# Optimization experiments

Hardware: AMD Instinct MI355X
Metric: run time of the kernel (lower is better)

The kernel has to match this reference:

```python
import jax, jax.numpy as jnp
import numpy as np

Q, N, H, C, L = 512, 1000, 1024, 128, 8  # questions, students, hidden, concepts, lstm layers
LAM, GUESS = 10.0, 0.25  # self.l and guess_prob


def setup_inputs() -> dict:
    key = jax.random.key(0)
    ks = jax.random.split(key, 12)
    def w(k, shape, fan):
        return (jax.random.uniform(k, shape, jnp.float32, -1.0, 1.0) / np.sqrt(fan)).astype(jnp.float32)
    return {
        "inputs": jax.random.normal(ks[0], (Q, N), jnp.float32),
        "concept_col": jax.random.randint(ks[1], (Q,), 0, C),  # concepts[1][i]
        "W_inp": w(ks[2], (H, N), N),
        "b_inp": jnp.zeros((H,), jnp.float32),
        "W_ih0": w(ks[3], (4 * N, H), H),
        "W_hh0": w(ks[4], (4 * N, N), N),
        "b_ih0": jnp.zeros((4 * N,), jnp.float32),
        "b_hh0": jnp.zeros((4 * N,), jnp.float32),
        "W_ih": w(ks[5], (L - 1, 4 * N, N), N),
        "W_hh": w(ks[6], (L - 1, 4 * N, N), N),
        "b_ih": jnp.zeros((L - 1, 4 * N), jnp.float32),
        "b_hh": jnp.zeros((L - 1, 4 * N), jnp.float32),
        "W_lin": w(ks[7], (C,), 1),  # Linear(1, C) weight, shape [C]
        "b_lin": jnp.zeros((C,), jnp.float32),
        "D_nz": 0.1 * jax.random.normal(ks[8], (Q,), jnp.float32),  # D[concepts]
    }


def _cell(Wih, Whh, bih, bhh, x, h, c):
    # PyTorch LSTM cell, gate order i,f,g,o
    g = Wih @ x + bih + Whh @ h + bhh
    i, f, gg, o = jnp.split(g, 4)
    i, f, o = jax.nn.sigmoid(i), jax.nn.sigmoid(f), jax.nn.sigmoid(o)
    c = f * c + i * jnp.tanh(gg)
    return o * jnp.tanh(c), c


def _forward(inputs, concept_col, W_inp, b_inp, W_ih0, W_hh0, b_ih0, b_hh0,
             W_ih, W_hh, b_ih, b_hh, W_lin, b_lin, D_nz):
    def step(carry, xs):
        h, c, ssum = carry  # h,c: [L,N]
        x_row, cc, d = xs
        x = W_inp @ x_row + b_inp  # [H]
        hs, cs = [], []
        hl, cl = _cell(W_ih0, W_hh0, b_ih0, b_hh0, x, h[0], c[0])
        hs.append(hl); cs.append(cl)
        for l in range(L - 1):
            hl, cl = _cell(W_ih[l], W_hh[l], b_ih[l], b_hh[l], hl, h[l + 1], c[l + 1])
            hs.append(hl); cs.append(cl)
        skills = hl[:, None] * W_lin[None, :] + b_lin  # [N, C]
        skills = (skills - skills.min()) / (skills.max() - skills.min())  # global min-max
        out = jnp.maximum(GUESS, 1.0 - jnp.exp(-LAM * (skills[:, cc] - d)))  # floored_exp_irf, [N]
        return (jnp.stack(hs), jnp.stack(cs), ssum + skills), out

    h0 = jnp.zeros((L, N), inputs.dtype)
    c0 = jnp.zeros((L, N), inputs.dtype)
    s0 = jnp.zeros((N, C), inputs.dtype)
    (h, c, ssum), outputs = jax.lax.scan(step, (h0, c0, s0), (inputs, concept_col, D_nz))
    return outputs, ssum / Q  # outputs [Q,N], averaged skills [N,C]


def reference(inputs, concept_col, W_inp, b_inp, W_ih0, W_hh0, b_ih0, b_hh0,
              W_ih, W_hh, b_ih, b_hh, W_lin, b_lin, D_nz):
    return _forward(inputs, concept_col, W_inp, b_inp, W_ih0, W_hh0, b_ih0, b_hh0,
                    W_ih, W_hh, b_ih, b_hh, W_lin, b_lin, D_nz)
```

## Files before the change

kernel.cpp:

```cpp
#include <hip/hip_runtime.h>
#include <math.h>

#define QQ 512
#define NN 1000
#define HHID 1024
#define HPAD 1024
#define CCON 128
#define G4 4000
#define LAYERS 8
#define TC 64
#define CHUNKS (QQ / TC)
#define CONC 4
#define LBLK 63
#define MAXSTG 32

typedef unsigned long long ull;

__device__ inline float wred_min(float v){ for(int o=32;o;o>>=1) v=fminf(v,__shfl_xor(v,o)); return v; }
__device__ inline float wred_max(float v){ for(int o=32;o;o>>=1) v=fmaxf(v,__shfl_xor(v,o)); return v; }
__device__ inline float wred_sum(float v){ for(int o=32;o;o>>=1) v+=__shfl_xor(v,o); return v; }

__global__ __launch_bounds__(256) void gemm_nt(
    const float* __restrict__ A, const float* __restrict__ B,
    const float* __restrict__ bias1,
    float* __restrict__ C, int M, int K, int R, int lda, int ldc) {
  __shared__ float As[16][65];
  __shared__ float Bs[16][65];
  int tid = threadIdx.x;
  int tx = tid & 15, ty = tid >> 4;
  int m0 = blockIdx.y * 64, r0 = blockIdx.x * 64;
  float acc[4][4] = {};
  for (int k0 = 0; k0 < K; k0 += 16) {
#pragma unroll
    for (int i = 0; i < 4; i++) {
      int idx = tid + 256 * i;
      int ml = idx >> 4, kl = idx & 15;
      int m = m0 + ml, k = k0 + kl;
      As[kl][ml] = (m < M && k < K) ? A[(size_t)m * lda + k] : 0.f;
      int r = r0 + ml;
      Bs[kl][ml] = (r < R && k < K) ? B[(size_t)r * K + k] : 0.f;
    }
    __syncthreads();
#pragma unroll
    for (int kk = 0; kk < 16; kk++) {
      float a[4], b[4];
#pragma unroll
      for (int i = 0; i < 4; i++) a[i] = As[kk][ty * 4 + i];
#pragma unroll
      for (int j = 0; j < 4; j++) b[j] = Bs[kk][tx * 4 + j];
#pragma unroll
      for (int i = 0; i < 4; i++)
#pragma unroll
        for (int j = 0; j < 4; j++) acc[i][j] += a[i] * b[j];
    }
    __syncthreads();
  }
#pragma unroll
  for (int i = 0; i < 4; i++) {
    int m = m0 + ty * 4 + i;
    if (m >= M) continue;
#pragma unroll
    for (int j = 0; j < 4; j++) {
      int r = r0 + tx * 4 + j;
      if (r >= R) continue;
      float v = acc[i][j];
      if (bias1) v += bias1[r];
      C[(size_t)m * ldc + r] = v;
    }
  }
}

struct PArgs {
  const float* X;
  const float* Wih0; const float* Whh0; const float* bih0; const float* bhh0;
  const float* Wih7; const float* Whh7; const float* bih7; const float* bhh7;
  ull* Hall; ull* Call64;
  int nstages;
  int pl[MAXSTG * CONC]; int pc[MAXSTG * CONC];
};

__global__ __launch_bounds__(1024, 4) void lstm_persist(PArgs a) {
  __shared__ __align__(16) float As[64][68];
  __shared__ __align__(16) float Bs[64][68];
  __shared__ float gl[TC * 64];
  __shared__ float hs[2][1024];
  int blkid = blockIdx.x;
  int lanePair = blockIdx.y;
  int tid = threadIdx.x;
  int wave = tid >> 6, lane = tid & 63;
  int n = blkid * 16 + wave;
  bool active = (n < NN);

  if (tid >= NN) { hs[0][tid] = 0.f; hs[1][tid] = 0.f; }
  __syncthreads();

  for (int s = 0; s < a.nstages; s++) {
    int l = a.pl[s * CONC + lanePair];
    if (l < 0) continue;
    int c = a.pc[s * CONC + lanePair];
    int t0 = c * TC;
    int kin = (l == 0) ? HHID : NN;
    const float* Wih = (l == 0) ? a.Wih0 : a.Wih7 + (size_t)(l - 1) * G4 * NN;
    const float* Whh = (l == 0) ? a.Whh0 : a.Whh7 + (size_t)(l - 1) * G4 * NN;
    const float* b1  = (l == 0) ? a.bih0 : a.bih7 + (size_t)(l - 1) * G4;
    const float* b2  = (l == 0) ? a.bhh0 : a.bhh7 + (size_t)(l - 1) * G4;
    const ull* Hin64 = a.Hall + (size_t)(l - 1) * QQ * HPAD;
    ull* Hout64 = a.Hall + (size_t)l * QQ * HPAD;
    ull* CallL = a.Call64 + (size_t)l * HPAD;

    if (l > 0) {
      if (tid < NN) {
        const ull* gp = &Hin64[(size_t)(t0 + TC - 1) * HPAD + tid];
        while ((unsigned)(__hip_atomic_load(gp, __ATOMIC_RELAXED,
                                            __HIP_MEMORY_SCOPE_AGENT) >> 32)
               != (unsigned)(t0 + TC))
          __builtin_amdgcn_s_sleep(8);
      }
      __syncthreads();
    }

    {
      int ttA = tid >> 4;
      int w16 = tid & 15;
      int nn = blkid * 16 + w16;
      float accq[4] = {0.f, 0.f, 0.f, 0.f};
      float pbq[4];
#pragma unroll
      for (int q = 0; q < 4; q++)
        pbq[q] = (nn < NN) ? b1[q * NN + nn] + b2[q * NN + nn] : 0.f;
      int ldr = tid >> 4, ldc4 = tid & 15;
      int qb = ldr >> 4, nb = blkid * 16 + (ldr & 15);
      for (int k0 = 0; k0 < kin; k0 += 64) {
        int k = k0 + ldc4 * 4;
        float4 av;
        if (l == 0) {
          av = *(const float4*)&a.X[(size_t)(t0 + ldr) * HPAD + k];
        } else {
          float f0 = 0.f, f1 = 0.f, f2 = 0.f, f3 = 0.f;
          const ull* rowp = &Hin64[(size_t)(t0 + ldr) * HPAD];
          if (k < kin)
            f0 = __uint_as_float((unsigned)__hip_atomic_load(
                &rowp[k], __ATOMIC_RELAXED, __HIP_MEMORY_SCOPE_AGENT));
          if (k + 1 < kin)
            f1 = __uint_as_float((unsigned)__hip_atomic_load(
                &rowp[k + 1], __ATOMIC_RELAXED, __HIP_MEMORY_SCOPE_AGENT));
          if (k + 2 < kin)
            f2 = __uint_as_float((unsigned)__hip_atomic_load(
                &rowp[k + 2], __ATOMIC_RELAXED, __HIP_MEMORY_SCOPE_AGENT));
          if (k + 3 < kin)
            f3 = __uint_as_float((unsigned)__hip_atomic_load(
                &rowp[k + 3], __ATOMIC_RELAXED, __HIP_MEMORY_SCOPE_AGENT));
          av.x = f0; av.y = f1; av.z = f2; av.w = f3;
        }
        *(float4*)&As[ldr][ldc4 * 4] = av;
        float4 bv = {0.f, 0.f, 0.f, 0.f};
        if (nb < NN) {
          if (k + 3 < kin) {
            bv = *(const float4*)&Wih[(size_t)(qb * NN + nb) * kin + k];
          } else {
            float* f = (float*)&bv;
#pragma unroll
            for (int e = 0; e < 4; e++)
              if (k + e < kin) f[e] = Wih[(size_t)(qb * NN + nb) * kin + k + e];
          }
        }
        *(float4*)&Bs[ldr][ldc4 * 4] = bv;
        __syncthreads();
#pragma unroll
        for (int kk = 0; kk < 64; kk += 4) {
          float4 aa = *(const float4*)&As[ttA][kk];
#pragma unroll
          for (int q = 0; q < 4; q++) {
            float4 b = *(const float4*)&Bs[q * 16 + w16][kk];
            accq[q] += aa.x * b.x + aa.y * b.y + aa.z * b.z + aa.w * b.w;
          }
        }
        __syncthreads();
      }
#pragma unroll
      for (int q = 0; q < 4; q++)
        gl[ttA * 64 + q * 16 + w16] = accq[q] + pbq[q];
    }

    float wreg[4][16];
    if (active) {
#pragma unroll
      for (int q = 0; q < 4; q++) {
        const float* wr = Whh + (size_t)(q * NN + n) * NN;
#pragma unroll
        for (int it = 0; it < 16; it++) {
          int k = it * 64 + lane;
          wreg[q][it] = (k < NN) ? wr[k] : 0.f;
        }
      }
    } else {
#pragma unroll
      for (int q = 0; q < 4; q++)
#pragma unroll
        for (int it = 0; it < 16; it++) wreg[q][it] = 0.f;
    }
#pragma unroll
    for (int q = 0; q < 4; q++)
#pragma unroll
      for (int it = 0; it < 16; it++)
        asm volatile("" : "+v"(wreg[q][it]));

    __syncthreads();

    float creg = 0.f;
    if (t0 > 0 && active) {
      const ull* cp = &CallL[n];
      for (;;) {
        ull v = __hip_atomic_load(cp, __ATOMIC_RELAXED,
                                  __HIP_MEMORY_SCOPE_AGENT);
        if ((unsigned)(v >> 32) == (unsigned)c) {
          creg = __uint_as_float((unsigned)v);
          break;
        }
        __builtin_amdgcn_s_sleep(2);
      }
    }

    for (int tt = 0; tt < TC; tt++) {
      int t = t0 + tt;
      float* hb = hs[t & 1];
      if (t > 0 && tid < NN) {
        const ull* src = Hout64 + (size_t)(t - 1) * HPAD + tid;
        for (;;) {
          ull v = __hip_atomic_load(src, __ATOMIC_RELAXED,
                                    __HIP_MEMORY_SCOPE_AGENT);
          if ((unsigned)(v >> 32) == (unsigned)t) {
            hb[tid] = __uint_as_float((unsigned)v);
            break;
          }
          __builtin_amdgcn_s_sleep(1);
        }
      }
      __syncthreads();
      if (active) {
        float g0 = gl[tt * 64 + wave];
        float g1 = gl[tt * 64 + 16 + wave];
        float g2 = gl[tt * 64 + 32 + wave];
        float g3 = gl[tt * 64 + 48 + wave];
        if (t > 0) {
          float a0 = 0.f, a1 = 0.f, a2 = 0.f, a3 = 0.f;
#pragma unroll
          for (int it = 0; it < 16; it++) {
            float hv = hb[it * 64 + lane];
            a0 += wreg[0][it] * hv;
            a1 += wreg[1][it] * hv;
            a2 += wreg[2][it] * hv;
            a3 += wreg[3][it] * hv;
          }
#pragma unroll
          for (int o = 32; o; o >>= 1) {
            a0 += __shfl_xor(a0, o);
            a1 += __shfl_xor(a1, o);
            a2 += __shfl_xor(a2, o);
            a3 += __shfl_xor(a3, o);
          }
          g0 += a0; g1 += a1; g2 += a2; g3 += a3;
        }
        float ii = 1.f / (1.f + expf(-g0));
        float ff = 1.f / (1.f + expf(-g1));
        float gg = tanhf(g2);
        float oo = 1.f / (1.f + expf(-g3));
        creg = ff * creg + ii * gg;
        float h = oo * tanhf(creg);
        if (lane == 0) {
          ull pkt = ((ull)(unsigned)(t + 1) << 32) | (ull)__float_as_uint(h);
          __hip_atomic_store(&Hout64[(size_t)t * HPAD + n], pkt,
                             __ATOMIC_RELAXED, __HIP_MEMORY_SCOPE_AGENT);
        }
      }
    }
    if (active && lane == 0) {
      ull pkt = ((ull)(unsigned)(c + 1) << 32) | (ull)__float_as_uint(creg);
      __hip_atomic_store(&CallL[n], pkt, __ATOMIC_RELAXED,
                         __HIP_MEMORY_SCOPE_AGENT);
    }
    __syncthreads();
  }
}

__global__ __launch_bounds__(256) void epilogue_out(
    const ull* __restrict__ H7,
    const float* __restrict__ Wlin, const float* __restrict__ blin,
    const int* __restrict__ ccol, const float* __restrict__ Dnz,
    float* __restrict__ out,
    float* __restrict__ irbuf, float* __restrict__ mnirbuf) {
  int t = blockIdx.x, tid = threadIdx.x;
  int wave = tid >> 6, lane = tid & 63;
  __shared__ float hbuf[NN];
  __shared__ float smin[4], smax[4];
  __shared__ float bc[2];
  float lmin = 3.4e38f, lmax = -3.4e38f;
  for (int i = tid; i < NN; i += 256) {
    float v = __uint_as_float((unsigned)H7[(size_t)t * HPAD + i]);
    hbuf[i] = v;
    lmin = fminf(lmin, v); lmax = fmaxf(lmax, v);
  }
  lmin = wred_min(lmin); lmax = wred_max(lmax);
  if (lane == 0) { smin[wave] = lmin; smax[wave] = lmax; }
  __syncthreads();
  if (tid == 0) {
    bc[0] = fminf(fminf(smin[0], smin[1]), fminf(smin[2], smin[3]));
    bc[1] = fmaxf(fmaxf(smax[0], smax[1]), fmaxf(smax[2], smax[3]));
  }
  __syncthreads();
  float hmn = bc[0], hmx = bc[1];
  float clo = 3.4e38f, chi = -3.4e38f;
  if (tid < CCON) {
    float w = Wlin[tid], b = blin[tid];
    clo = b + fminf(w * hmn, w * hmx);
    chi = b + fmaxf(w * hmn, w * hmx);
  }
  clo = wred_min(clo); chi = wred_max(chi);
  __syncthreads();
  if (lane == 0) { smin[wave] = clo; smax[wave] = chi; }
  __syncthreads();
  if (tid == 0) {
    float mn = fminf(fminf(smin[0], smin[1]), fminf(smin[2], smin[3]));
    float mx = fmaxf(fmaxf(smax[0], smax[1]), fmaxf(smax[2], smax[3]));
    float ir = 1.f / (mx - mn);
    bc[0] = mn; bc[1] = ir;
    irbuf[t] = ir;
    mnirbuf[t] = mn * ir;
  }
  __syncthreads();
  float mn = bc[0], ir = bc[1];
  int cc = ccol[t];
  float wcc = Wlin[cc], bcc = blin[cc], d = Dnz[t];
  for (int n = tid; n < NN; n += 256) {
    float s = (hbuf[n] * wcc + bcc - mn) * ir;
    out[(size_t)t * NN + n] = fmaxf(0.25f, 1.f - expf(-10.f * (s - d)));
  }
}

__global__ void reduce_scalars(const float* __restrict__ ir,
                               const float* __restrict__ mnir,
                               float* __restrict__ scal) {
  int tid = threadIdx.x;
  int wave = tid >> 6, lane = tid & 63;
  __shared__ float s1[8], s2[8];
  float a = ir[tid], b = mnir[tid];
  a = wred_sum(a); b = wred_sum(b);
  if (lane == 0) { s1[wave] = a; s2[wave] = b; }
  __syncthreads();
  if (tid == 0) {
    float A = 0.f, B = 0.f;
    for (int i = 0; i < 8; i++) { A += s1[i]; B += s2[i]; }
    scal[0] = A; scal[1] = B;
  }
}

__global__ void accum_A(const ull* __restrict__ H7,
                        const float* __restrict__ ir,
                        float* __restrict__ Avec) {
  int n = blockIdx.x * 256 + threadIdx.x;
  if (n < NN) {
    float acc = 0.f;
    for (int t = 0; t < QQ; t++)
      acc += __uint_as_float((unsigned)H7[(size_t)t * HPAD + n]) * ir[t];
    Avec[n] = acc;
  }
}

__global__ void skills_out(const float* __restrict__ Avec,
                           const float* __restrict__ Wlin,
                           const float* __restrict__ blin,
                           const float* __restrict__ scal,
                           float* __restrict__ out) {
  int idx = blockIdx.x * 256 + threadIdx.x;
  if (idx < NN * CCON) {
    int n = idx >> 7, c = idx & 127;
    out[idx] = (Wlin[c] * Avec[n] + blin[c] * scal[0] - scal[1]) * (1.f / (float)QQ);
  }
}

extern "C" void kernel_launch(void* const* d_in, const int* in_sizes, int n_in,
                              void* d_out, int out_size, void* d_ws, size_t ws_size,
                              hipStream_t stream) {
  const float* inputs = (const float*)d_in[0];
  const int*   ccol   = (const int*)d_in[1];
  const float* W_inp  = (const float*)d_in[2];
  const float* b_inp  = (const float*)d_in[3];
  const float* W_ih0  = (const float*)d_in[4];
  const float* W_hh0  = (const float*)d_in[5];
  const float* b_ih0  = (const float*)d_in[6];
  const float* b_hh0  = (const float*)d_in[7];
  const float* W_ih   = (const float*)d_in[8];
  const float* W_hh   = (const float*)d_in[9];
  const float* b_ih   = (const float*)d_in[10];
  const float* b_hh   = (const float*)d_in[11];
  const float* W_lin  = (const float*)d_in[12];
  const float* b_lin  = (const float*)d_in[13];
  const float* D_nz   = (const float*)d_in[14];

  float* ws = (float*)d_ws;
  float* X     = ws;
  ull*   Hall  = (ull*)(X + (size_t)QQ * HPAD);
  ull*   Call64 = Hall + (size_t)LAYERS * QQ * HPAD;
  float* tail  = (float*)(Call64 + (size_t)LAYERS * HPAD);
  float* irb   = tail;
  float* mnir  = irb + QQ;
  float* Avec  = mnir + QQ;
  float* scal  = Avec + 1024;

  float* out_main   = (float*)d_out;
  float* out_skills = (float*)d_out + QQ * NN;

  hipMemsetAsync(Hall, 0,
                 ((size_t)LAYERS * QQ * HPAD + LAYERS * HPAD) * sizeof(ull),
                 stream);

  gemm_nt<<<dim3(HPAD / 64, QQ / 64), 256, 0, stream>>>(
      inputs, W_inp, b_inp, X, QQ, NN, HPAD, NN, HPAD);

  PArgs pa;
  pa.X = X;
  pa.Wih0 = W_ih0; pa.Whh0 = W_hh0; pa.bih0 = b_ih0; pa.bhh0 = b_hh0;
  pa.Wih7 = W_ih; pa.Whh7 = W_hh; pa.bih7 = b_ih; pa.bhh7 = b_hh;
  pa.Hall = Hall; pa.Call64 = Call64;
  for (int i = 0; i < MAXSTG * CONC; i++) { pa.pl[i] = -1; pa.pc[i] = -1; }
  {
    bool donep[LAYERS][CHUNKS] = {};
    int remaining = LAYERS * CHUNKS;
    int s = 0;
    while (remaining > 0 && s < MAXSTG) {
      bool sel[LAYERS][CHUNKS] = {};
      int np = 0;
      int spl[CONC], spc[CONC];
      for (int pick = 0; pick < CONC; pick++) {
        int bl = -1, bc = -1, bkey = 1 << 30;
        for (int l = 0; l < LAYERS; l++)
          for (int c = 0; c < CHUNKS; c++) {
            if (donep[l][c] || sel[l][c]) continue;
            if (l > 0 && !donep[l - 1][c]) continue;
            if (c > 0 && !donep[l][c - 1]) continue;
            int key = (l + c) * 16 + (LAYERS - 1 - l);
            if (key < bkey) { bkey = key; bl = l; bc = c; }
          }
        if (bl < 0) break;
        sel[bl][bc] = true; spl[np] = bl; spc[np] = bc; np++;
      }
      for (int i = 0; i < np; i++) {
        pa.pl[s * CONC + i] = spl[i];
        pa.pc[s * CONC + i] = spc[i];
        donep[spl[i]][spc[i]] = true;
      }
      remaining -= np;
      s++;
    }
    pa.nstages = s;
  }
  lstm_persist<<<dim3(LBLK, CONC), 1024, 0, stream>>>(pa);

  const ull* H7 = Hall + (size_t)7 * QQ * HPAD;
  epilogue_out<<<QQ, 256, 0, stream>>>(H7, W_lin, b_lin, ccol, D_nz,
                                       out_main, irb, mnir);
  reduce_scalars<<<1, 512, 0, stream>>>(irb, mnir, scal);
  accum_A<<<4, 256, 0, stream>>>(H7, irb, Avec);
  skills_out<<<(NN * CCON) / 256, 256, 0, stream>>>(Avec, W_lin, b_lin, scal,
                                                    out_skills);
}
```

Before: 7.200 ms.

## Replace host-planned wavefront schedule with fixed layer-to-lane assignment

Drops the host-computed stage table that assigned (layer, chunk) tiles to four block lanes. Each lane now owns layers j and j+4 and walks all chunks in order, so the cell state stays in a register and the Call64 handoff buffer and its memset go away. The input projection is split into two 32-row halves that each wait only for their own rows of the previous layer, which lets a layer start sooner. The trade-off is that only half the threads do FMAs in the projection and the fixed pairing of layers may leave lanes idle during pipeline fill and drain.

New measurement: 8.220 ms. 14.2% more time.

```diff
diff --git a/kernel.cpp b/kernel.cpp
--- a/kernel.cpp
+++ b/kernel.cpp
@@ -10,9 +10,8 @@
 #define LAYERS 8
 #define TC 64
 #define CHUNKS (QQ / TC)
-#define CONC 4
+#define NLANE 4
 #define LBLK 63
-#define MAXSTG 32
 
 typedef unsigned long long ull;
 
@@ -74,18 +73,16 @@
   const float* X;
   const float* Wih0; const float* Whh0; const float* bih0; const float* bhh0;
   const float* Wih7; const float* Whh7; const float* bih7; const float* bhh7;
-  ull* Hall; ull* Call64;
-  int nstages;
-  int pl[MAXSTG * CONC]; int pc[MAXSTG * CONC];
+  ull* Hall;
 };
 
-__global__ __launch_bounds__(1024, 4) void lstm_persist(PArgs a) {
-  __shared__ __align__(16) float As[64][68];
+__global__ __launch_bounds__(1024, 4) void lstm_resident(PArgs a) {
+  __shared__ __align__(16) float As[32][68];
   __shared__ __align__(16) float Bs[64][68];
   __shared__ float gl[TC * 64];
   __shared__ float hs[2][1024];
+  int j = blockIdx.y;
   int blkid = blockIdx.x;
-  int lanePair = blockIdx.y;
   int tid = threadIdx.x;
   int wave = tid >> 6, lane = tid & 63;
   int n = blkid * 16 + wave;
@@ -94,11 +91,10 @@
   if (tid >= NN) { hs[0][tid] = 0.f; hs[1][tid] = 0.f; }
   __syncthreads();
 
-  for (int s = 0; s < a.nstages; s++) {
-    int l = a.pl[s * CONC + lanePair];
-    if (l < 0) continue;
-    int c = a.pc[s * CONC + lanePair];
-    int t0 = c * TC;
+  float creg = 0.f;
+
+  for (int seq = 0; seq < 2; seq++) {
+    int l = j + 4 * seq;
     int kin = (l == 0) ? HHID : NN;
     const float* Wih = (l == 0) ? a.Wih0 : a.Wih7 + (size_t)(l - 1) * G4 * NN;
     const float* Whh = (l == 0) ? a.Whh0 : a.Whh7 + (size_t)(l - 1) * G4 * NN;
@@ -106,180 +102,170 @@
     const float* b2  = (l == 0) ? a.bhh0 : a.bhh7 + (size_t)(l - 1) * G4;
     const ull* Hin64 = a.Hall + (size_t)(l - 1) * QQ * HPAD;
     ull* Hout64 = a.Hall + (size_t)l * QQ * HPAD;
-    ull* CallL = a.Call64 + (size_t)l * HPAD;
-
-    if (l > 0) {
-      if (tid < NN) {
-        const ull* gp = &Hin64[(size_t)(t0 + TC - 1) * HPAD + tid];
-        while ((unsigned)(__hip_atomic_load(gp, __ATOMIC_RELAXED,
-                                            __HIP_MEMORY_SCOPE_AGENT) >> 32)
-               != (unsigned)(t0 + TC))
-          __builtin_amdgcn_s_sleep(8);
+
+    for (int c = 0; c < CHUNKS; c++) {
+      int t0 = c * TC;
+      if (c == 0) creg = 0.f;
+
+      for (int g = 0; g < 2; g++) {
+        int r0 = t0 + 32 * g;
+        if (l > 0) {
+          if (tid < NN) {
+            const ull* gp = &Hin64[(size_t)(r0 + 31) * HPAD + tid];
+            while ((unsigned)(__hip_atomic_load(gp, __ATOMIC_RELAXED,
+                                                __HIP_MEMORY_SCOPE_AGENT) >> 32)
+                   != (unsigned)(r0 + 32))
+              __builtin_amdgcn_s_sleep(4);
+          }
+          __syncthreads();
+        }
+        int ttA = tid >> 4;
+        int w16 = tid & 15;
+        bool act = (tid < 512);
+        int nn = blkid * 16 + w16;
+        float accq[4] = {0.f, 0.f, 0.f, 0.f};
+        float pbq[4];
+#pragma unroll
+        for (int q = 0; q < 4; q++)
+          pbq[q] = (nn < NN) ? b1[q * NN + nn] + b2[q * NN + nn] : 0.f;
+        int arow = tid >> 5, ac2 = (tid & 31) * 2;
+        int brow = tid >> 4, bc4 = (tid & 15) * 4;
+        int qb = brow >> 4, nb = blkid * 16 + (brow & 15);
+        for (int k0 = 0; k0 < kin; k0 += 64) {
+          if (l == 0) {
+            const float* rowp = &a.X[(size_t)(r0 + arow) * HPAD + k0];
+            As[arow][ac2]     = rowp[ac2];
+            As[arow][ac2 + 1] = rowp[ac2 + 1];
+          } else {
+            const ull* rowp = &Hin64[(size_t)(r0 + arow) * HPAD + k0];
+            int ka = k0 + ac2;
+            As[arow][ac2] = (ka < kin)
+                ? __uint_as_float((unsigned)__hip_atomic_load(
+                      &rowp[ac2], __ATOMIC_RELAXED, __HIP_MEMORY_SCOPE_AGENT))
+                : 0.f;
+            As[arow][ac2 + 1] = (ka + 1 < kin)
+                ? __uint_as_float((unsigned)__hip_atomic_load(
+                      &rowp[ac2 + 1], __ATOMIC_RELAXED,
+                      __HIP_MEMORY_SCOPE_AGENT))
+                : 0.f;
+          }
+          {
+            int k = k0 + bc4;
+            float4 bv = {0.f, 0.f, 0.f, 0.f};
+            if (nb < NN) {
+              if (k + 3 < kin) {
+                bv = *(const float4*)&Wih[(size_t)(qb * NN + nb) * kin + k];
+              } else {
+                float* f = (float*)&bv;
+#pragma unroll
+                for (int e = 0; e < 4; e++)
+                  if (k + e < kin)
+                    f[e] = Wih[(size_t)(qb * NN + nb) * kin + k + e];
+              }
+            }
+            *(float4*)&Bs[brow][bc4] = bv;
+          }
+          __syncthreads();
+          if (act) {
+#pragma unroll
+            for (int kk = 0; kk < 64; kk += 4) {
+              float4 av = *(const float4*)&As[ttA][kk];
+#pragma unroll
+              for (int q = 0; q < 4; q++) {
+                float4 b = *(const float4*)&Bs[q * 16 + w16][kk];
+                accq[q] += av.x * b.x + av.y * b.y + av.z * b.z + av.w * b.w;
+              }
+            }
+          }
+          __syncthreads();
+        }
+        if (act) {
+#pragma unroll
+          for (int q = 0; q < 4; q++)
+            gl[(32 * g + ttA) * 64 + q * 16 + w16] = accq[q] + pbq[q];
+        }
+      }
+
+      float wreg[4][16];
+      if (active) {
+#pragma unroll
+        for (int q = 0; q < 4; q++) {
+          const float* wr = Whh + (size_t)(q * NN + n) * NN;
+#pragma unroll
+          for (int it = 0; it < 16; it++) {
+            int k = it * 64 + lane;
+            wreg[q][it] = (k < NN) ? wr[k] : 0.f;
+          }
+        }
+      } else {
+#pragma unroll
+        for (int q = 0; q < 4; q++)
+#pragma unroll
+          for (int it = 0; it < 16; it++) wreg[q][it] = 0.f;
+      }
+#pragma unroll
+      for (int q = 0; q < 4; q++)
+#pragma unroll
+        for (int it = 0; it < 16; it++)
+          asm volatile("" : "+v"(wreg[q][it]));
+
+      __syncthreads();
+
+      for (int tt = 0; tt < TC; tt++) {
+        int t = t0 + tt;
+        float* hb = hs[t & 1];
+        if (t > 0 && tid < NN) {
+          const ull* src = Hout64 + (size_t)(t - 1) * HPAD + tid;
+          for (;;) {
+            ull v = __hip_atomic_load(src, __ATOMIC_RELAXED,
+                                      __HIP_MEMORY_SCOPE_AGENT);
+            if ((unsigned)(v >> 32) == (unsigned)t) {
+              hb[tid] = __uint_as_float((unsigned)v);
+              break;
+            }
+            __builtin_amdgcn_s_sleep(1);
+          }
+        }
+        __syncthreads();
+        if (active) {
+          float g0 = gl[tt * 64 + wave];
+          float g1 = gl[tt * 64 + 16 + wave];
+          float g2 = gl[tt * 64 + 32 + wave];
+          float g3 = gl[tt * 64 + 48 + wave];
+          if (t > 0) {
+            float a0 = 0.f, a1 = 0.f, a2 = 0.f, a3 = 0.f;
+#pragma unroll
+            for (int it = 0; it < 16; it++) {
+              float hv = hb[it * 64 + lane];
+              a0 += wreg[0][it] * hv;
+              a1 += wreg[1][it] * hv;
+              a2 += wreg[2][it] * hv;
+              a3 += wreg[3][it] * hv;
+            }
+#pragma unroll
+            for (int o = 32; o; o >>= 1) {
+              a0 += __shfl_xor(a0, o);
+              a1 += __shfl_xor(a1, o);
+              a2 += __shfl_xor(a2, o);
+              a3 += __shfl_xor(a3, o);
+            }
+            g0 += a0; g1 += a1; g2 += a2; g3 += a3;
+          }
+          float ii = 1.f / (1.f + expf(-g0));
+          float ff = 1.f / (1.f + expf(-g1));
+          float gg = tanhf(g2);
+          float oo = 1.f / (1.f + expf(-g3));
+          creg = ff * creg + ii * gg;
+          float h = oo * tanhf(creg);
+          if (lane == 0) {
+            ull pkt = ((ull)(unsigned)(t + 1) << 32) | (ull)__float_as_uint(h);
+            __hip_atomic_store(&Hout64[(size_t)t * HPAD + n], pkt,
+                               __ATOMIC_RELAXED, __HIP_MEMORY_SCOPE_AGENT);
+          }
+        }
       }
       __syncthreads();
     }
-
-    {
-      int ttA = tid >> 4;
-      int w16 = tid & 15;
-      int nn = blkid * 16 + w16;
-      float accq[4] = {0.f, 0.f, 0.f, 0.f};
-      float pbq[4];
-#pragma unroll
-      for (int q = 0; q < 4; q++)
-        pbq[q] = (nn < NN) ? b1[q * NN + nn] + b2[q * NN + nn] : 0.f;
-      int ldr = tid >> 4, ldc4 = tid & 15;
-      int qb = ldr >> 4, nb = blkid * 16 + (ldr & 15);
-      for (int k0 = 0; k0 < kin; k0 += 64) {
-        int k = k0 + ldc4 * 4;
-        float4 av;
-        if (l == 0) {
-          av = *(const float4*)&a.X[(size_t)(t0 + ldr) * HPAD + k];
-        } else {
-          float f0 = 0.f, f1 = 0.f, f2 = 0.f, f3 = 0.f;
-          const ull* rowp = &Hin64[(size_t)(t0 + ldr) * HPAD];
-          if (k < kin)
-            f0 = __uint_as_float((unsigned)__hip_atomic_load(
-                &rowp[k], __ATOMIC_RELAXED, __HIP_MEMORY_SCOPE_AGENT));
-          if (k + 1 < kin)
-            f1 = __uint_as_float((unsigned)__hip_atomic_load(
-                &rowp[k + 1], __ATOMIC_RELAXED, __HIP_MEMORY_SCOPE_AGENT));
-          if (k + 2 < kin)
-            f2 = __uint_as_float((unsigned)__hip_atomic_load(
-                &rowp[k + 2], __ATOMIC_RELAXED, __HIP_MEMORY_SCOPE_AGENT));
-          if (k + 3 < kin)
-            f3 = __uint_as_float((unsigned)__hip_atomic_load(
-                &rowp[k + 3], __ATOMIC_RELAXED, __HIP_MEMORY_SCOPE_AGENT));
-          av.x = f0; av.y = f1; av.z = f2; av.w = f3;
-        }
-        *(float4*)&As[ldr][ldc4 * 4] = av;
-        float4 bv = {0.f, 0.f, 0.f, 0.f};
-        if (nb < NN) {
-          if (k + 3 < kin) {
-            bv = *(const float4*)&Wih[(size_t)(qb * NN + nb) * kin + k];
-          } else {
-            float* f = (float*)&bv;
-#pragma unroll
-            for (int e = 0; e < 4; e++)
-              if (k + e < kin) f[e] = Wih[(size_t)(qb * NN + nb) * kin + k + e];
-          }
-        }
-        *(float4*)&Bs[ldr][ldc4 * 4] = bv;
-        __syncthreads();
-#pragma unroll
-        for (int kk = 0; kk < 64; kk += 4) {
-          float4 aa = *(const float4*)&As[ttA][kk];
-#pragma unroll
-          for (int q = 0; q < 4; q++) {
-            float4 b = *(const float4*)&Bs[q * 16 + w16][kk];
-            accq[q] += aa.x * b.x + aa.y * b.y + aa.z * b.z + aa.w * b.w;
-          }
-        }
-        __syncthreads();
-      }
-#pragma unroll
-      for (int q = 0; q < 4; q++)
-        gl[ttA * 64 + q * 16 + w16] = accq[q] + pbq[q];
-    }
-
-    float wreg[4][16];
-    if (active) {
-#pragma unroll
-      for (int q = 0; q < 4; q++) {
-        const float* wr = Whh + (size_t)(q * NN + n) * NN;
-#pragma unroll
-        for (int it = 0; it < 16; it++) {
-          int k = it * 64 + lane;
-          wreg[q][it] = (k < NN) ? wr[k] : 0.f;
-        }
-      }
-    } else {
-#pragma unroll
-      for (int q = 0; q < 4; q++)
-#pragma unroll
-        for (int it = 0; it < 16; it++) wreg[q][it] = 0.f;
-    }
-#pragma unroll
-    for (int q = 0; q < 4; q++)
-#pragma unroll
-      for (int it = 0; it < 16; it++)
-        asm volatile("" : "+v"(wreg[q][it]));
-
-    __syncthreads();
-
-    float creg = 0.f;
-    if (t0 > 0 && active) {
-      const ull* cp = &CallL[n];
-      for (;;) {
-        ull v = __hip_atomic_load(cp, __ATOMIC_RELAXED,
-                                  __HIP_MEMORY_SCOPE_AGENT);
-        if ((unsigned)(v >> 32) == (unsigned)c) {
-          creg = __uint_as_float((unsigned)v);
-          break;
-        }
-        __builtin_amdgcn_s_sleep(2);
-      }
-    }
-
-    for (int tt = 0; tt < TC; tt++) {
-      int t = t0 + tt;
-      float* hb = hs[t & 1];
-      if (t > 0 && tid < NN) {
-        const ull* src = Hout64 + (size_t)(t - 1) * HPAD + tid;
-        for (;;) {
-          ull v = __hip_atomic_load(src, __ATOMIC_RELAXED,
-                                    __HIP_MEMORY_SCOPE_AGENT);
-          if ((unsigned)(v >> 32) == (unsigned)t) {
-            hb[tid] = __uint_as_float((unsigned)v);
-            break;
-          }
-          __builtin_amdgcn_s_sleep(1);
-        }
-      }
-      __syncthreads();
-      if (active) {
-        float g0 = gl[tt * 64 + wave];
-        float g1 = gl[tt * 64 + 16 + wave];
-        float g2 = gl[tt * 64 + 32 + wave];
-        float g3 = gl[tt * 64 + 48 + wave];
-        if (t > 0) {
-          float a0 = 0.f, a1 = 0.f, a2 = 0.f, a3 = 0.f;
-#pragma unroll
-          for (int it = 0; it < 16; it++) {
-            float hv = hb[it * 64 + lane];
-            a0 += wreg[0][it] * hv;
-            a1 += wreg[1][it] * hv;
-            a2 += wreg[2][it] * hv;
-            a3 += wreg[3][it] * hv;
-          }
-#pragma unroll
-          for (int o = 32; o; o >>= 1) {
-            a0 += __shfl_xor(a0, o);
-            a1 += __shfl_xor(a1, o);
-            a2 += __shfl_xor(a2, o);
-            a3 += __shfl_xor(a3, o);
-          }
-          g0 += a0; g1 += a1; g2 += a2; g3 += a3;
-        }
-        float ii = 1.f / (1.f + expf(-g0));
-        float ff = 1.f / (1.f + expf(-g1));
-        float gg = tanhf(g2);
-        float oo = 1.f / (1.f + expf(-g3));
-        creg = ff * creg + ii * gg;
-        float h = oo * tanhf(creg);
-        if (lane == 0) {
-          ull pkt = ((ull)(unsigned)(t + 1) << 32) | (ull)__float_as_uint(h);
-          __hip_atomic_store(&Hout64[(size_t)t * HPAD + n], pkt,
-                             __ATOMIC_RELAXED, __HIP_MEMORY_SCOPE_AGENT);
-        }
-      }
-    }
-    if (active && lane == 0) {
-      ull pkt = ((ull)(unsigned)(c + 1) << 32) | (ull)__float_as_uint(creg);
-      __hip_atomic_store(&CallL[n], pkt, __ATOMIC_RELAXED,
-                         __HIP_MEMORY_SCOPE_AGENT);
-    }
-    __syncthreads();
   }
 }
 
@@ -400,8 +386,7 @@
   float* ws = (float*)d_ws;
   float* X     = ws;
   ull*   Hall  = (ull*)(X + (size_t)QQ * HPAD);
-  ull*   Call64 = Hall + (size_t)LAYERS * QQ * HPAD;
-  float* tail  = (float*)(Call64 + (size_t)LAYERS * HPAD);
+  float* tail  = (float*)(Hall + (size_t)LAYERS * QQ * HPAD);
   float* irb   = tail;
   float* mnir  = irb + QQ;
   float* Avec  = mnir + QQ;
@@ -410,9 +395,7 @@
   float* out_main   = (float*)d_out;
   float* out_skills = (float*)d_out + QQ * NN;
 
-  hipMemsetAsync(Hall, 0,
-                 ((size_t)LAYERS * QQ * HPAD + LAYERS * HPAD) * sizeof(ull),
-                 stream);
+  hipMemsetAsync(Hall, 0, (size_t)LAYERS * QQ * HPAD * sizeof(ull), stream);
 
   gemm_nt<<<dim3(HPAD / 64, QQ / 64), 256, 0, stream>>>(
       inputs, W_inp, b_inp, X, QQ, NN, HPAD, NN, HPAD);
@@ -421,40 +404,8 @@
   pa.X = X;
   pa.Wih0 = W_ih0; pa.Whh0 = W_hh0; pa.bih0 = b_ih0; pa.bhh0 = b_hh0;
   pa.Wih7 = W_ih; pa.Whh7 = W_hh; pa.bih7 = b_ih; pa.bhh7 = b_hh;
-  pa.Hall = Hall; pa.Call64 = Call64;
-  for (int i = 0; i < MAXSTG * CONC; i++) { pa.pl[i] = -1; pa.pc[i] = -1; }
-  {
-    bool donep[LAYERS][CHUNKS] = {};
-    int remaining = LAYERS * CHUNKS;
-    int s = 0;
-    while (remaining > 0 && s < MAXSTG) {
-      bool sel[LAYERS][CHUNKS] = {};
-      int np = 0;
-      int spl[CONC], spc[CONC];
-      for (int pick = 0; pick < CONC; pick++) {
-        int bl = -1, bc = -1, bkey = 1 << 30;
-        for (int l = 0; l < LAYERS; l++)
-          for (int c = 0; c < CHUNKS; c++) {
-            if (donep[l][c] || sel[l][c]) continue;
-            if (l > 0 && !donep[l - 1][c]) continue;
-            if (c > 0 && !donep[l][c - 1]) continue;
-            int key = (l + c) * 16 + (LAYERS - 1 - l);
-            if (key < bkey) { bkey = key; bl = l; bc = c; }
-          }
-        if (bl < 0) break;
-        sel[bl][bc] = true; spl[np] = bl; spc[np] = bc; np++;
-      }
-      for (int i = 0; i < np; i++) {
-        pa.pl[s * CONC + i] = spl[i];
-        pa.pc[s * CONC + i] = spc[i];
-        donep[spl[i]][spc[i]] = true;
-      }
-      remaining -= np;
-      s++;
-    }
-    pa.nstages = s;
-  }
-  lstm_persist<<<dim3(LBLK, CONC), 1024, 0, stream>>>(pa);
+  pa.Hall = Hall;
+  lstm_resident<<<dim3(LBLK, NLANE), 1024, 0, stream>>>(pa);
 
   const ull* H7 = Hall + (size_t)7 * QQ * HPAD;
   epilogue_out<<<QQ, 256, 0, stream>>>(H7, W_lin, b_lin, ccol, D_nz,
```
